# Kernel tuning notes

Hardware: AMD Instinct MI355X
Metric: run time of the kernel (lower is better)

Reference implementation:

```python
import jax, jax.numpy as jnp
import numpy as np
import math

B, C, H, W = 8, 256, 64, 64
CQK = C // 8

def _conv1x1(x, w, b):
    # x: [B,C,H,W], w: [O,C], b: [O]  (1x1 conv == per-pixel linear)
    return jnp.einsum('bchw,oc->bohw', x, w) + b[None, :, None, None]

def setup_inputs() -> dict:
    key = jax.random.key(0)
    ks = jax.random.split(key, 7)
    inputs = jax.random.normal(ks[0], (B, C, H, W), dtype=jnp.float32)
    # init_weight: normal(0, sqrt(2/(k*k*out_channels))) for 1x1 convs
    wq = jax.random.normal(ks[1], (CQK, C), dtype=jnp.float32) * math.sqrt(2.0 / CQK)
    wk = jax.random.normal(ks[2], (CQK, C), dtype=jnp.float32) * math.sqrt(2.0 / CQK)
    wv = jax.random.normal(ks[3], (C, C), dtype=jnp.float32) * math.sqrt(2.0 / C)
    bq = jnp.zeros((CQK,), dtype=jnp.float32)
    bk = jnp.zeros((CQK,), dtype=jnp.float32)
    bv = jnp.zeros((C,), dtype=jnp.float32)
    # torch init is zeros(1); use nonzero so the attention path contributes
    alpha = jnp.full((1,), 0.5, dtype=jnp.float32)
    return {"inputs": inputs, "wq": wq, "bq": bq, "wk": wk, "bk": bk,
            "wv": wv, "bv": bv, "alpha": alpha}

def reference(inputs, wq, bq, wk, bk, wv, bv, alpha):
    b, c, h, w = inputs.shape
    n = h * w
    q = _conv1x1(inputs, wq, bq).reshape(b, -1, n)          # [B, C/8, N]
    k = _conv1x1(inputs, wk, bk).reshape(b, -1, n)          # [B, C/8, N]
    v = _conv1x1(inputs, wv, bv).reshape(b, c, n)           # [B, C, N]
    # attention_weight[b, i, j] = q[:, i] . k[:, j]
    attn = jnp.einsum('bdi,bdj->bij', q, k)                 # [B, N, N]
    attn = jax.nn.softmax(attn, axis=-1)
    # value @ attn^T : out[b, c, i] = sum_j v[b, c, j] * attn[b, i, j]
    out = jnp.einsum('bcj,bij->bci', v, attn)               # [B, C, N]
    return alpha[0] * out.reshape(inputs.shape) + inputs
```

## Files before the change

### kernel.cpp

```cpp
#include <hip/hip_runtime.h>
#include <math.h>

#define B_  8
#define C_  256
#define N_  4096
#define NJC (N_ / 128)
#define PLD 136
#define LOG2E 1.4426950408889634f

using frag  = __attribute__((ext_vector_type(8))) short;
using f32x4 = __attribute__((ext_vector_type(4))) float;

__device__ __forceinline__ unsigned short f2bf(float f) {
    unsigned u = __float_as_uint(f);
    u += 0x7fffu + ((u >> 16) & 1u);
    return (unsigned short)(u >> 16);
}
__device__ __forceinline__ float bf2f(unsigned short h) {
    return __uint_as_float(((unsigned)h) << 16);
}
#define PK2(a, b) (((unsigned)(a)) | (((unsigned)(b)) << 16))

__device__ __forceinline__ f32x4 fmax4(f32x4 a, f32x4 b) {
    f32x4 r;
    r[0] = fmaxf(a[0], b[0]); r[1] = fmaxf(a[1], b[1]);
    r[2] = fmaxf(a[2], b[2]); r[3] = fmaxf(a[3], b[3]);
    return r;
}

__device__ __forceinline__ float exp2_raw(float x) {
    float r;
    asm("v_exp_f32 %0, %1" : "=v"(r) : "v"(x));
    return r;
}

__global__ __launch_bounds__(256) void wprep_kernel(
    const float* __restrict__ wq, const float* __restrict__ wk,
    const float* __restrict__ wv,
    unsigned short* __restrict__ whf, unsigned short* __restrict__ wlf)
{
    const int fid  = blockIdx.x * 256 + threadIdx.x;
    if (fid >= 20 * 8 * 64) return;
    const int g    = fid >> 9;
    const int kc   = (fid >> 6) & 7;
    const int lane = fid & 63;
    const int r16  = lane & 15, q = lane >> 4;

    const float* src; int row;
    if (g < 2)      { src = wq; row = g * 16 + r16; }
    else if (g < 4) { src = wk; row = (g - 2) * 16 + r16; }
    else            { src = wv; row = (g - 4) * 16 + r16; }

    const float scl = (g < 2) ? LOG2E : 1.0f;
    const float* wp = src + row * 256 + kc * 32 + q * 8;
    float v[8];
#pragma unroll
    for (int j = 0; j < 8; ++j) v[j] = wp[j] * scl;

    unsigned short h[8];
#pragma unroll
    for (int j = 0; j < 8; ++j) h[j] = f2bf(v[j]);
    uint4 U;
    U.x = PK2(h[0], h[1]); U.y = PK2(h[2], h[3]);
    U.z = PK2(h[4], h[5]); U.w = PK2(h[6], h[7]);
    *(uint4*)&whf[(size_t)fid * 8] = U;

    if (g < 4) {
        unsigned short l[8];
#pragma unroll
        for (int j = 0; j < 8; ++j) l[j] = f2bf(v[j] - bf2f(h[j]));
        uint4 V;
        V.x = PK2(l[0], l[1]); V.y = PK2(l[2], l[3]);
        V.z = PK2(l[4], l[5]); V.w = PK2(l[6], l[7]);
        *(uint4*)&wlf[(size_t)fid * 8] = V;
    }
}

__global__ __launch_bounds__(256, 4) void proj_kernel(
    const float* __restrict__ x,
    const float* __restrict__ bq, const float* __restrict__ bk,
    const float* __restrict__ bv,
    const unsigned short* __restrict__ whf, const unsigned short* __restrict__ wlf,
    unsigned short* __restrict__ qh, unsigned short* __restrict__ ql,
    unsigned short* __restrict__ kh, unsigned short* __restrict__ kl,
    unsigned short* __restrict__ vbf)
{
    __shared__ unsigned xpk[32 * 260 + 4];

    const int tid  = threadIdx.x;
    const int w    = tid >> 6;
    const int lane = tid & 63;
    const int quad = lane >> 4;
    const int l16  = lane & 15;
    const int n0   = blockIdx.x * 32;
    const int b    = blockIdx.y;

    {
        const int p  = tid & 31;
        const int cb = tid >> 5;
        const float* xbase = x + (size_t)b * C_ * N_ + n0 + p;
#pragma unroll 16
        for (int s = 0; s < 32; ++s) {
            const int c = s * 8 + cb;
            const float v = xbase[(size_t)c * N_];
            const unsigned short hb = f2bf(v);
            const unsigned short lb = f2bf(v - bf2f(hb));
            xpk[p * 260 + c] = (((unsigned)hb) << 16) | lb;
        }
    }
    __syncthreads();

    const frag* wh = (const frag*)whf;
    const frag* wl = (const frag*)wlf;

    f32x4 aqk[2];
    f32x4 av[4][2];
#pragma unroll
    for (int ps = 0; ps < 2; ++ps) {
        aqk[ps] = (f32x4){0.f, 0.f, 0.f, 0.f};
#pragma unroll
        for (int vg = 0; vg < 4; ++vg) av[vg][ps] = (f32x4){0.f, 0.f, 0.f, 0.f};
    }

    for (int kc = 0; kc < 8; ++kc) {
        const frag ah = wh[(w * 8 + kc) * 64 + lane];
        const frag al = wl[(w * 8 + kc) * 64 + lane];
        frag avw[4];
#pragma unroll
        for (int vg = 0; vg < 4; ++vg)
            avw[vg] = wh[((4 + w * 4 + vg) * 8 + kc) * 64 + lane];

#pragma unroll
        for (int ps = 0; ps < 2; ++ps) {
            const unsigned* row = &xpk[(ps * 16 + l16) * 260 + kc * 32 + quad * 8];
            const uint4 A  = *(const uint4*)row;
            const uint4 Bv = *(const uint4*)(row + 4);
            frag bh, bl;
            unsigned* bhp = (unsigned*)&bh;
            unsigned* blp = (unsigned*)&bl;
            bhp[0] = __builtin_amdgcn_perm(A.y,  A.x,  0x07060302u);
            bhp[1] = __builtin_amdgcn_perm(A.w,  A.z,  0x07060302u);
            bhp[2] = __builtin_amdgcn_perm(Bv.y, Bv.x, 0x07060302u);
            bhp[3] = __builtin_amdgcn_perm(Bv.w, Bv.z, 0x07060302u);
            blp[0] = __builtin_amdgcn_perm(A.y,  A.x,  0x05040100u);
            blp[1] = __builtin_amdgcn_perm(A.w,  A.z,  0x05040100u);
            blp[2] = __builtin_amdgcn_perm(Bv.y, Bv.x, 0x05040100u);
            blp[3] = __builtin_amdgcn_perm(Bv.w, Bv.z, 0x05040100u);

            aqk[ps] = __builtin_amdgcn_mfma_f32_16x16x32_bf16(ah, bh, aqk[ps], 0, 0, 0);
            aqk[ps] = __builtin_amdgcn_mfma_f32_16x16x32_bf16(al, bh, aqk[ps], 0, 0, 0);
            aqk[ps] = __builtin_amdgcn_mfma_f32_16x16x32_bf16(ah, bl, aqk[ps], 0, 0, 0);
#pragma unroll
            for (int vg = 0; vg < 4; ++vg)
                av[vg][ps] = __builtin_amdgcn_mfma_f32_16x16x32_bf16(
                    avw[vg], bh, av[vg][ps], 0, 0, 0);
        }
    }

    {
        const bool isq = (w < 2);
        const float* bias = isq ? bq : bk;
        const float bscl = isq ? LOG2E : 1.0f;
        const int dbase = (isq ? w : w - 2) * 16 + quad * 4;
        unsigned short* dsth = isq ? qh : kh;
        unsigned short* dstl = isq ? ql : kl;
        float bvals[4];
#pragma unroll
        for (int r = 0; r < 4; ++r) bvals[r] = bias[dbase + r] * bscl;
#pragma unroll
        for (int ps = 0; ps < 2; ++ps) {
            const int n = n0 + ps * 16 + l16;
            unsigned short hs[4], ls[4];
#pragma unroll
            for (int r = 0; r < 4; ++r) {
                const float f = aqk[ps][r] + bvals[r];
                hs[r] = f2bf(f);
                ls[r] = f2bf(f - bf2f(hs[r]));
            }
            const size_t off = ((size_t)(b * N_ + n)) * 32 + dbase;
            *(uint2*)&dsth[off] = make_uint2(PK2(hs[0], hs[1]), PK2(hs[2], hs[3]));
            *(uint2*)&dstl[off] = make_uint2(PK2(ls[0], ls[1]), PK2(ls[2], ls[3]));
        }
    }
#pragma unroll
    for (int vg = 0; vg < 4; ++vg)
#pragma unroll
        for (int ps = 0; ps < 2; ++ps) {
            const int n = n0 + ps * 16 + l16;
#pragma unroll
            for (int r = 0; r < 4; ++r) {
                const int c = (w * 4 + vg) * 16 + quad * 4 + r;
                vbf[((size_t)b * C_ + c) * N_ + n] = f2bf(av[vg][ps][r] + bv[c]);
            }
        }
}

__global__ __launch_bounds__(512, 2) void attn_kernel(
    const unsigned short* __restrict__ qh, const unsigned short* __restrict__ ql,
    const unsigned short* __restrict__ khg, const unsigned short* __restrict__ klg,
    const unsigned short* __restrict__ vbf,
    const float* __restrict__ x, const float* __restrict__ alpha_p,
    float* __restrict__ out)
{
    __shared__ __align__(16) short kbuf[2][2][128 * 32];
    __shared__ __align__(16) short p_s[2][128 * PLD];
    __shared__ float alpha_s[2][128];
    __shared__ float l_s[128];

    const int tid  = threadIdx.x;
    const int w    = tid >> 6;
    const int lane = tid & 63;
    const int quad = lane >> 4;
    const int l16  = lane & 15;
    const int bid  = blockIdx.x;
    const int b    = bid & 7;
    const int i0   = (bid >> 3) * 128;

    const size_t qoff = ((size_t)(b * N_ + i0 + w * 16 + l16)) * 32 + quad * 8;
    const frag qhf = *(const frag*)(qh + qoff);
    const frag qlf = *(const frag*)(ql + qoff);

    const unsigned short* khb = khg + (size_t)b * N_ * 32;
    const unsigned short* klb = klg + (size_t)b * N_ * 32;
    const unsigned short* vb  = vbf + (size_t)b * C_ * N_;

    f32x4 o[8][2];
#pragma unroll
    for (int it = 0; it < 8; ++it) {
        o[it][0] = (f32x4){0.f, 0.f, 0.f, 0.f};
        o[it][1] = (f32x4){0.f, 0.f, 0.f, 0.f};
    }

    float m_run = -INFINITY, l_run = 0.f;

    const int r_st  = w * 16 + l16;
    const int qc_st = quad;
    const int gsto  = r_st * 32 + qc_st * 8;
    const int lsto  = qc_st * 1024 + r_st * 8;

    frag vf[4][2];

    {
        const uint4 h0 = *(const uint4*)(khb + gsto);
        const uint4 l0 = *(const uint4*)(klb + gsto);
        *(uint4*)&kbuf[0][0][lsto] = h0;
        *(uint4*)&kbuf[0][1][lsto] = l0;
    }
    __syncthreads();

    for (int jc = 0; jc < NJC; ++jc) {
        const int bf = jc & 1;

        f32x4 st[8];
#pragma unroll
        for (int js = 0; js < 8; ++js) {
            const frag ka  = *(const frag*)&kbuf[bf][0][quad * 1024 + (js * 16 + l16) * 8];
            const frag kb2 = *(const frag*)&kbuf[bf][1][quad * 1024 + (js * 16 + l16) * 8];
            f32x4 s = (f32x4){0.f, 0.f, 0.f, 0.f};
            s = __builtin_amdgcn_mfma_f32_16x16x32_bf16(ka, qhf, s, 0, 0, 0);
            s = __builtin_amdgcn_mfma_f32_16x16x32_bf16(ka, qlf, s, 0, 0, 0);
            s = __builtin_amdgcn_mfma_f32_16x16x32_bf16(kb2, qhf, s, 0, 0, 0);
            st[js] = s;
        }

        const int jn = (jc + 1 < NJC) ? jc + 1 : jc;
        const uint4 knh = *(const uint4*)(khb + (size_t)jn * 4096 + gsto);
        const uint4 knl = *(const uint4*)(klb + (size_t)jn * 4096 + gsto);

        if (jc > 0) {
#pragma unroll
            for (int it = 0; it < 8; ++it)
#pragma unroll
                for (int r = 0; r < 4; ++r) {
                    const float al = alpha_s[bf ^ 1][it * 16 + quad * 4 + r];
                    o[it][0][r] *= al;
                    o[it][1][r] *= al;
                }
#pragma unroll
            for (int ks = 0; ks < 4; ++ks) {
#pragma unroll
                for (int it = 0; it < 8; ++it) {
                    const frag pf = *(const frag*)&p_s[bf ^ 1][(it * 16 + l16) * PLD
                                                              + ks * 32 + quad * 8];
                    o[it][0] = __builtin_amdgcn_mfma_f32_16x16x32_bf16(pf, vf[ks][0], o[it][0], 0, 0, 0);
                    o[it][1] = __builtin_amdgcn_mfma_f32_16x16x32_bf16(pf, vf[ks][1], o[it][1], 0, 0, 0);
                }
            }
        }

#pragma unroll
        for (int ks = 0; ks < 4; ++ks)
#pragma unroll
            for (int ct = 0; ct < 2; ++ct)
                vf[ks][ct] = *(const frag*)(vb
                    + (size_t)(w * 32 + ct * 16 + l16) * N_
                    + jc * 128 + ks * 32 + quad * 8);

        f32x4 t0 = fmax4(fmax4(st[0], st[1]), fmax4(st[2], st[3]));
        f32x4 t1 = fmax4(fmax4(st[4], st[5]), fmax4(st[6], st[7]));
        t0 = fmax4(t0, t1);
        float mx = fmaxf(fmaxf(t0[0], t0[1]), fmaxf(t0[2], t0[3]));
        mx = fmaxf(mx, __shfl_xor(mx, 16));
        mx = fmaxf(mx, __shfl_xor(mx, 32));
        const float mnew = fmaxf(m_run, mx);
        const float sc   = exp2_raw(m_run - mnew);

        f32x4 ps4 = (f32x4){0.f, 0.f, 0.f, 0.f};
#pragma unroll
        for (int js = 0; js < 8; ++js) {
#pragma unroll
            for (int r = 0; r < 4; ++r) st[js][r] = exp2_raw(st[js][r] - mnew);
            ps4[0] += st[js][0]; ps4[1] += st[js][1];
            ps4[2] += st[js][2]; ps4[3] += st[js][3];
        }
        float ps = (ps4[0] + ps4[1]) + (ps4[2] + ps4[3]);
        ps += __shfl_xor(ps, 16);
        ps += __shfl_xor(ps, 32);
        l_run = l_run * sc + ps;
        m_run = mnew;
        if (quad == 0) alpha_s[bf][w * 16 + l16] = sc;

#pragma unroll
        for (int js = 0; js < 8; ++js) {
            const unsigned a0 = __float_as_uint(st[js][0]) + 0x8000u;
            const unsigned a1 = __float_as_uint(st[js][1]) + 0x8000u;
            const unsigned a2 = __float_as_uint(st[js][2]) + 0x8000u;
            const unsigned a3 = __float_as_uint(st[js][3]) + 0x8000u;
            const unsigned p01 = __builtin_amdgcn_perm(a1, a0, 0x07060302u);
            const unsigned p23 = __builtin_amdgcn_perm(a3, a2, 0x07060302u);
            *(uint2*)&p_s[bf][(w * 16 + l16) * PLD + js * 16 + quad * 4] =
                make_uint2(p01, p23);
        }

        *(uint4*)&kbuf[bf ^ 1][0][lsto] = knh;
        *(uint4*)&kbuf[bf ^ 1][1][lsto] = knl;

        __syncthreads();
    }

    {
        const int bl = (NJC - 1) & 1;
#pragma unroll
        for (int it = 0; it < 8; ++it)
#pragma unroll
            for (int r = 0; r < 4; ++r) {
                const float al = alpha_s[bl][it * 16 + quad * 4 + r];
                o[it][0][r] *= al;
                o[it][1][r] *= al;
            }
#pragma unroll
        for (int ks = 0; ks < 4; ++ks) {
#pragma unroll
            for (int it = 0; it < 8; ++it) {
                const frag pf = *(const frag*)&p_s[bl][(it * 16 + l16) * PLD
                                                       + ks * 32 + quad * 8];
                o[it][0] = __builtin_amdgcn_mfma_f32_16x16x32_bf16(pf, vf[ks][0], o[it][0], 0, 0, 0);
                o[it][1] = __builtin_amdgcn_mfma_f32_16x16x32_bf16(pf, vf[ks][1], o[it][1], 0, 0, 0);
            }
        }
    }

    if (quad == 0) l_s[w * 16 + l16] = l_run;
    __syncthreads();
    const float av = alpha_p[0];

#pragma unroll
    for (int it = 0; it < 8; ++it) {
        float invl[4];
#pragma unroll
        for (int r = 0; r < 4; ++r) invl[r] = 1.f / l_s[it * 16 + quad * 4 + r];
#pragma unroll
        for (int ct = 0; ct < 2; ++ct) {
            const int c = w * 32 + ct * 16 + l16;
            const size_t base = (size_t)b * C_ * N_ + (size_t)c * N_
                                + i0 + it * 16 + quad * 4;
            const float4 xv = *(const float4*)(x + base);
            float4 ov;
            ov.x = av * (o[it][ct][0] * invl[0]) + xv.x;
            ov.y = av * (o[it][ct][1] * invl[1]) + xv.y;
            ov.z = av * (o[it][ct][2] * invl[2]) + xv.z;
            ov.w = av * (o[it][ct][3] * invl[3]) + xv.w;
            *(float4*)(out + base) = ov;
        }
    }
}

extern "C" void kernel_launch(void* const* d_in, const int* in_sizes, int n_in,
                              void* d_out, int out_size, void* d_ws, size_t ws_size,
                              hipStream_t stream)
{
    const float* x  = (const float*)d_in[0];
    const float* wq = (const float*)d_in[1];
    const float* bq = (const float*)d_in[2];
    const float* wk = (const float*)d_in[3];
    const float* bk = (const float*)d_in[4];
    const float* wv = (const float*)d_in[5];
    const float* bv = (const float*)d_in[6];
    const float* al = (const float*)d_in[7];
    float* out = (float*)d_out;

    char* ws = (char*)d_ws;
    unsigned short* qh  = (unsigned short*)(ws + 0);
    unsigned short* ql  = (unsigned short*)(ws + (size_t)2  * 1024 * 1024);
    unsigned short* kh  = (unsigned short*)(ws + (size_t)4  * 1024 * 1024);
    unsigned short* kl  = (unsigned short*)(ws + (size_t)6  * 1024 * 1024);
    unsigned short* vbf = (unsigned short*)(ws + (size_t)8  * 1024 * 1024);
    unsigned short* whf = (unsigned short*)(ws + (size_t)24 * 1024 * 1024);
    unsigned short* wlf = (unsigned short*)(ws + (size_t)24 * 1024 * 1024 + 256 * 1024);

    wprep_kernel<<<40, 256, 0, stream>>>(wq, wk, wv, whf, wlf);
    proj_kernel<<<dim3(N_ / 32, B_), 256, 0, stream>>>(
        x, bq, bk, bv, whf, wlf, qh, ql, kh, kl, vbf);
    attn_kernel<<<dim3(256), 512, 0, stream>>>(
        qh, ql, kh, kl, vbf, x, al, out);
}
```

Baseline: 207.2 us.

## Retile PV accumulation per wave to 64 rows by 64 channels

Changes the split of the P·V output across the 8 waves from 128 query rows × 32 channels to a 2×4 grid of 64 query rows × 64 channels. Each wave now loads half as many P fragments from LDS per V fragment and reuses each P fragment across four channel tiles. The MFMA count per wave stays the same. The cost is that each wave loads twice as many V fragments from global memory (vf grows to 4×4), which raises register pressure. Alpha and l values are now read as vectorized f32x4 LDS loads.

```diff
diff --git a/kernel.cpp b/kernel.cpp
--- a/kernel.cpp
+++ b/kernel.cpp
@@ -204,8 +204,8 @@
 {
     __shared__ __align__(16) short kbuf[2][2][128 * 32];
     __shared__ __align__(16) short p_s[2][128 * PLD];
-    __shared__ float alpha_s[2][128];
-    __shared__ float l_s[128];
+    __shared__ __align__(16) float alpha_s[2][128];
+    __shared__ __align__(16) float l_s[128];
 
     const int tid  = threadIdx.x;
     const int w    = tid >> 6;
@@ -215,6 +215,8 @@
     const int bid  = blockIdx.x;
     const int b    = bid & 7;
     const int i0   = (bid >> 3) * 128;
+    const int wi   = w >> 2;
+    const int wc   = w & 3;
 
     const size_t qoff = ((size_t)(b * N_ + i0 + w * 16 + l16)) * 32 + quad * 8;
     const frag qhf = *(const frag*)(qh + qoff);
@@ -224,12 +226,12 @@
     const unsigned short* klb = klg + (size_t)b * N_ * 32;
     const unsigned short* vb  = vbf + (size_t)b * C_ * N_;
 
-    f32x4 o[8][2];
-#pragma unroll
-    for (int it = 0; it < 8; ++it) {
-        o[it][0] = (f32x4){0.f, 0.f, 0.f, 0.f};
-        o[it][1] = (f32x4){0.f, 0.f, 0.f, 0.f};
-    }
+    f32x4 o[4][4];
+#pragma unroll
+    for (int it = 0; it < 4; ++it)
+#pragma unroll
+        for (int ct = 0; ct < 4; ++ct)
+            o[it][ct] = (f32x4){0.f, 0.f, 0.f, 0.f};
 
     float m_run = -INFINITY, l_run = 0.f;
 
@@ -238,7 +240,7 @@
     const int gsto  = r_st * 32 + qc_st * 8;
     const int lsto  = qc_st * 1024 + r_st * 8;
 
-    frag vf[4][2];
+    frag vf[4][4];
 
     {
         const uint4 h0 = *(const uint4*)(khb + gsto);
@@ -269,21 +271,24 @@
 
         if (jc > 0) {
 #pragma unroll
-            for (int it = 0; it < 8; ++it)
+            for (int it = 0; it < 4; ++it) {
+                const f32x4 alf = *(const f32x4*)&alpha_s[bf ^ 1][wi * 64 + it * 16 + quad * 4];
 #pragma unroll
                 for (int r = 0; r < 4; ++r) {
-                    const float al = alpha_s[bf ^ 1][it * 16 + quad * 4 + r];
-                    o[it][0][r] *= al;
-                    o[it][1][r] *= al;
+#pragma unroll
+                    for (int ct = 0; ct < 4; ++ct) o[it][ct][r] *= alf[r];
                 }
+            }
 #pragma unroll
             for (int ks = 0; ks < 4; ++ks) {
 #pragma unroll
-                for (int it = 0; it < 8; ++it) {
-                    const frag pf = *(const frag*)&p_s[bf ^ 1][(it * 16 + l16) * PLD
+                for (int it = 0; it < 4; ++it) {
+                    const frag pf = *(const frag*)&p_s[bf ^ 1][(wi * 64 + it * 16 + l16) * PLD
                                                               + ks * 32 + quad * 8];
-                    o[it][0] = __builtin_amdgcn_mfma_f32_16x16x32_bf16(pf, vf[ks][0], o[it][0], 0, 0, 0);
-                    o[it][1] = __builtin_amdgcn_mfma_f32_16x16x32_bf16(pf, vf[ks][1], o[it][1], 0, 0, 0);
+#pragma unroll
+                    for (int ct = 0; ct < 4; ++ct)
+                        o[it][ct] = __builtin_amdgcn_mfma_f32_16x16x32_bf16(
+                            pf, vf[ks][ct], o[it][ct], 0, 0, 0);
                 }
             }
         }
@@ -291,9 +296,9 @@
 #pragma unroll
         for (int ks = 0; ks < 4; ++ks)
 #pragma unroll
-            for (int ct = 0; ct < 2; ++ct)
+            for (int ct = 0; ct < 4; ++ct)
                 vf[ks][ct] = *(const frag*)(vb
-                    + (size_t)(w * 32 + ct * 16 + l16) * N_
+                    + (size_t)(wc * 64 + ct * 16 + l16) * N_
                     + jc * 128 + ks * 32 + quad * 8);
 
         f32x4 t0 = fmax4(fmax4(st[0], st[1]), fmax4(st[2], st[3]));
@@ -341,21 +346,24 @@
     {
         const int bl = (NJC - 1) & 1;
 #pragma unroll
-        for (int it = 0; it < 8; ++it)
+        for (int it = 0; it < 4; ++it) {
+            const f32x4 alf = *(const f32x4*)&alpha_s[bl][wi * 64 + it * 16 + quad * 4];
 #pragma unroll
             for (int r = 0; r < 4; ++r) {
-                const float al = alpha_s[bl][it * 16 + quad * 4 + r];
-                o[it][0][r] *= al;
-                o[it][1][r] *= al;
-            }
+#pragma unroll
+                for (int ct = 0; ct < 4; ++ct) o[it][ct][r] *= alf[r];
+            }
+        }
 #pragma unroll
         for (int ks = 0; ks < 4; ++ks) {
 #pragma unroll
-            for (int it = 0; it < 8; ++it) {
-                const frag pf = *(const frag*)&p_s[bl][(it * 16 + l16) * PLD
+            for (int it = 0; it < 4; ++it) {
+                const frag pf = *(const frag*)&p_s[bl][(wi * 64 + it * 16 + l16) * PLD
                                                        + ks * 32 + quad * 8];
-                o[it][0] = __builtin_amdgcn_mfma_f32_16x16x32_bf16(pf, vf[ks][0], o[it][0], 0, 0, 0);
-                o[it][1] = __builtin_amdgcn_mfma_f32_16x16x32_bf16(pf, vf[ks][1], o[it][1], 0, 0, 0);
+#pragma unroll
+                for (int ct = 0; ct < 4; ++ct)
+                    o[it][ct] = __builtin_amdgcn_mfma_f32_16x16x32_bf16(
+                        pf, vf[ks][ct], o[it][ct], 0, 0, 0);
             }
         }
     }
@@ -365,15 +373,16 @@
     const float av = alpha_p[0];
 
 #pragma unroll
-    for (int it = 0; it < 8; ++it) {
+    for (int it = 0; it < 4; ++it) {
+        const f32x4 lv = *(const f32x4*)&l_s[wi * 64 + it * 16 + quad * 4];
         float invl[4];
 #pragma unroll
-        for (int r = 0; r < 4; ++r) invl[r] = 1.f / l_s[it * 16 + quad * 4 + r];
-#pragma unroll
-        for (int ct = 0; ct < 2; ++ct) {
-            const int c = w * 32 + ct * 16 + l16;
+        for (int r = 0; r < 4; ++r) invl[r] = 1.f / lv[r];
+#pragma unroll
+        for (int ct = 0; ct < 4; ++ct) {
+            const int c = wc * 64 + ct * 16 + l16;
             const size_t base = (size_t)b * C_ * N_ + (size_t)c * N_
-                                + i0 + it * 16 + quad * 4;
+                                + i0 + wi * 64 + it * 16 + quad * 4;
             const float4 xv = *(const float4*)(x + base);
             float4 ov;
             ov.x = av * (o[it][ct][0] * invl[0]) + xv.x;
```

After: 252.0 us. +21.6%, slower.
